# Kernel optimization log

Hardware: AMD Instinct MI355X
Metric: run time of the kernel (lower is better)

The kernel has to match this reference:

```python
import jax, jax.numpy as jnp
import numpy as np

N_NODES = 50000
N_EDGES = 800000
F_IN = 128
HID = 128
F_ADD = 32
N_GRAPHS = 128


def setup_inputs() -> dict:
    key = jax.random.key(0)
    ks = jax.random.split(key, 12)
    x = jax.random.normal(ks[0], (N_NODES, F_IN), dtype=jnp.float32)
    edge_index = jax.random.randint(ks[1], (2, N_EDGES), 0, N_NODES, dtype=jnp.int64)
    batch = jnp.sort(jax.random.randint(ks[2], (N_NODES,), 0, N_GRAPHS, dtype=jnp.int64))
    additional_features = jax.random.normal(ks[3], (N_GRAPHS, F_ADD), dtype=jnp.float32)
    def glorot(k, shape):
        fan_in, fan_out = shape[0], shape[1]
        lim = jnp.sqrt(6.0 / (fan_in + fan_out)).astype(jnp.float32)
        return jax.random.uniform(k, shape, jnp.float32, -lim, lim)
    W1 = glorot(ks[4], (F_IN, HID)); b1 = jnp.zeros((HID,), jnp.float32)
    W2 = glorot(ks[5], (HID, HID)); b2 = jnp.zeros((HID,), jnp.float32)
    fc1_w = glorot(ks[6], (HID + F_ADD, HID)); fc1_b = jnp.zeros((HID,), jnp.float32)
    fc2_w = glorot(ks[7], (HID, 2)); fc2_b = jnp.zeros((2,), jnp.float32)
    return {"x": x, "edge_index": edge_index, "batch": batch,
            "additional_features": additional_features,
            "W1": W1, "b1": b1, "W2": W2, "b2": b2,
            "fc1_w": fc1_w, "fc1_b": fc1_b, "fc2_w": fc2_w, "fc2_b": fc2_b}


def _gcn_conv(h, src, dst, norm, W, b):
    # h: [N, d_in]; symmetric-normalized scatter-add aggregation (PyG GCNConv)
    h = h @ W                                   # [N, d_out]
    msg = h[src] * norm[:, None]                # gather + scale: [E+N, d_out]
    return jax.ops.segment_sum(msg, dst, num_segments=N_NODES) + b


def reference(x, edge_index, batch, additional_features,
              W1, b1, W2, b2, fc1_w, fc1_b, fc2_w, fc2_b):
    loops = jnp.arange(N_NODES, dtype=edge_index.dtype)
    src = jnp.concatenate([edge_index[0], loops])   # A + I
    dst = jnp.concatenate([edge_index[1], loops])
    deg = jax.ops.segment_sum(jnp.ones_like(src, dtype=x.dtype), dst,
                              num_segments=N_NODES)
    dinv = jnp.where(deg > 0, jax.lax.rsqrt(jnp.maximum(deg, 1.0)), 0.0)
    norm = dinv[src] * dinv[dst]

    h = jax.nn.relu(_gcn_conv(x, src, dst, norm, W1, b1))
    h = jax.nn.relu(_gcn_conv(h, src, dst, norm, W2, b2))
    # dropout is identity in eval mode

    sums = jax.ops.segment_sum(h, batch, num_segments=N_GRAPHS)    # [G, HID]
    counts = jax.ops.segment_sum(jnp.ones((N_NODES,), h.dtype), batch,
                                 num_segments=N_GRAPHS)
    pooled = sums / jnp.maximum(counts, 1.0)[:, None]              # global_mean_pool

    z = jnp.concatenate([pooled, additional_features], axis=1)     # [G, HID+F_ADD]
    z = jax.nn.relu(z @ fc1_w + fc1_b)
    return z @ fc2_w + fc2_b                                       # [G, 2]
```

## Files before the change

kernel.cpp:

```cpp
#include <hip/hip_runtime.h>

#define NN 50000
#define NE 800000
#define FD 128
#define FDH 64
#define FA 32
#define NG 128
#define EETOT (NE + NN)
#define NBLK ((NN + 255) / 256)
#define FEPB 2048
#define FNCH ((EETOT + FEPB - 1) / FEPB)
#define NPXCD 6250

typedef __attribute__((ext_vector_type(8))) short short8;
typedef __attribute__((ext_vector_type(4))) float f32x4;

__device__ __forceinline__ float bfbits(unsigned short u) {
    return __uint_as_float(((unsigned int)u) << 16);
}
__device__ __forceinline__ float bflo(unsigned int p) { return __uint_as_float(p << 16); }
__device__ __forceinline__ float bfhi(unsigned int p) { return __uint_as_float(p & 0xffff0000u); }
__device__ __forceinline__ unsigned short f2bf(float f) {
    unsigned int u = __float_as_uint(f);
    unsigned int r = u + 0x7FFFu + ((u >> 16) & 1u);
    return (unsigned short)(r >> 16);
}
__device__ __forceinline__ unsigned int packbf(float a, float b) {
    return (unsigned int)f2bf(a) | ((unsigned int)f2bf(b) << 16);
}

__device__ __forceinline__ int wave_probe_bf16(const unsigned int* t, int nwords) {
    int lane = threadIdx.x & 63;
    unsigned int wv = (lane < nwords) ? t[lane] : 0u;
    int nzp = (wv != 0u) ? 1 : 0;
    unsigned int e = (wv >> 7) & 0xFFu;
    int hitp = (nzp && e >= 100u && e <= 140u) ? 1 : 0;
    int nz = __popcll(__ballot(nzp));
    int hits = __popcll(__ballot(hitp));
    return (nz < 8) ? 1 : (hits * 4 >= nz * 3);
}
__device__ __forceinline__ int wave_probe_is64(const int* ei) {
    int lane = threadIdx.x & 63;
    int v = (lane < 32) ? ei[2 * lane + 1] : 0;
    return (__ballot(v != 0) == 0ull) ? 1 : 0;
}

__global__ __launch_bounds__(128) void mark_kernel(float* out, float v) {
    out[threadIdx.x] = v;
}

__global__ __launch_bounds__(256) void prep(
        const void* addf, const void* w1, const void* b1, const void* w2,
        const void* b2, const void* fc1w, const void* fc1b, const void* fc2w,
        const void* fc2b, unsigned int* W1t, unsigned int* W2t,
        float* addff, float* b1f, float* b2f, float* fc1wf, float* fc1bf,
        float* fc2wf, float* fc2bf, int* degi, int* tsum, float* part) {
    int b = blockIdx.x;
    if (b < 64) {
        int rel = b * 256 + threadIdx.x;
        const void* src = (rel < 8192) ? w1 : w2;
        unsigned int* dst = (rel < 8192) ? W1t : W2t;
        int flag = wave_probe_bf16((const unsigned int*)src, 64);
        int rr = rel & 8191;
        int n = rr >> 6, kk = rr & 63;
        float lo, hi;
        if (flag) {
            const unsigned short* s = (const unsigned short*)src;
            lo = bfbits(s[(2 * kk) * FD + n]);
            hi = bfbits(s[(2 * kk + 1) * FD + n]);
        } else {
            const float* s = (const float*)src;
            lo = s[(2 * kk) * FD + n];
            hi = s[(2 * kk + 1) * FD + n];
        }
        dst[rr] = packbf(lo, hi);
    } else if (b < 163) {
        int i = (b - 64) * 256 + threadIdx.x;
        int wb = (b - 64) * 256 + (threadIdx.x & ~63);
        const void* src; float* dst; int base; int prnw; int lim;
        if      (wb < 4096)  { src = addf; dst = addff; base = 0;     prnw = 64; lim = 4096;  }
        else if (wb < 4224)  { src = b1;   dst = b1f;   base = 4096;  prnw = 64; lim = 128;   }
        else if (wb < 4352)  { src = b2;   dst = b2f;   base = 4224;  prnw = 64; lim = 128;   }
        else if (wb < 24832) { src = fc1w; dst = fc1wf; base = 4352;  prnw = 64; lim = 20480; }
        else if (wb < 24960) { src = fc1b; dst = fc1bf; base = 24832; prnw = 64; lim = 128;   }
        else if (wb < 25216) { src = fc2w; dst = fc2wf; base = 24960; prnw = 64; lim = 256;   }
        else if (wb < 25280) { src = fc2b; dst = fc2bf; base = 25216; prnw = 1;  lim = 2;     }
        else return;
        int flag = wave_probe_bf16((const unsigned int*)src, prnw);
        int rel = i - base;
        if (rel < lim) {
            if (flag) dst[rel] = bfbits(((const unsigned short*)src)[rel]);
            else      dst[rel] = ((const float*)src)[rel];
        }
    } else {
        int i = (b - 163) * 256 + threadIdx.x;
        if      (i < NN)            degi[i] = 0;
        else if (i < NN + 256)      tsum[i - NN] = 0;
        else if (i < NN + 256 + NG * FD) part[i - NN - 256] = 0.f;
    }
}

__global__ __launch_bounds__(256) void deg_kernel(const int* ei, int* deg,
                                                  int* s32, int* d32) {
    int is64 = wave_probe_is64(ei);
    int e = blockIdx.x * 256 + threadIdx.x;
    if (e < NE) {
        int s = is64 ? ei[2 * e] : ei[e];
        int d = is64 ? ei[2 * (NE + e)] : ei[NE + e];
        s32[e] = s;
        d32[e] = d;
        atomicAdd(&deg[d], 1);
    }
}

__global__ __launch_bounds__(256) void scan_fused(const int* degi, const int* batch,
        int* tsum, float* dinv, int* rowstart, int* cursor, int* gstart) {
    __shared__ int sh[256];
    int b = blockIdx.x, t = threadIdx.x;
    int i = b * 256 + t;
    int d = (i < NN) ? degi[i] : 0;
    if (i < NN) dinv[i] = rsqrtf((float)(d + 1));
    int v = (i < NN) ? d + 1 : 0;
    sh[t] = v;
    __syncthreads();
    for (int off = 1; off < 256; off <<= 1) {
        int a = (t >= off) ? sh[t - off] : 0;
        __syncthreads();
        sh[t] += a;
        __syncthreads();
    }
    int incl = sh[t];
    int total = sh[255];
    if (t == 0) atomicExch(&tsum[b], total);
    int pt = 0;
    for (int j = t; j < b; j += 256) {
        int s;
        do { s = atomicAdd(&tsum[j], 0); } while (s == 0);
        pt += s;
    }
    __syncthreads();
    sh[t] = pt;
    __syncthreads();
    for (int off = 128; off >= 1; off >>= 1) {
        if (t < off) sh[t] += sh[t + off];
        __syncthreads();
    }
    int boff = sh[0];
    if (i < NN) {
        int r = boff + incl - v;
        rowstart[i] = r;
        cursor[i]   = r;
    }
    if (i == 0) rowstart[NN] = EETOT;
    if (i < NN) {
        int is64 = (batch[NN - 1] == 0) ? 1 : 0;
        int bc = is64 ? batch[2 * i] : batch[i];
        if (i == 0) {
            for (int g = 0; g <= bc; ++g) gstart[g] = 0;
        } else {
            int bp = is64 ? batch[2 * (i - 1)] : batch[i - 1];
            for (int g = bp + 1; g <= bc; ++g) gstart[g] = i;
        }
        if (i == NN - 1) {
            for (int g = bc + 1; g <= NG; ++g) gstart[g] = NN;
        }
    }
}

__global__ __launch_bounds__(256) void fill_kernel(const int* s32, const int* d32,
        const float* dinv, int* cursor, unsigned int* cv) {
    int chunk = blockIdx.x >> 3;
    int par   = blockIdx.x & 7;
    int base  = chunk * FEPB;
    #pragma unroll
    for (int k = 0; k < FEPB / 256; ++k) {
        int e = base + k * 256 + threadIdx.x;
        if (e >= EETOT) break;
        int s, d;
        if (e < NE) { d = d32[e]; s = -1; }
        else        { s = d = e - NE; }
        if (d / NPXCD != par) continue;
        if (s < 0) s = s32[e];
        int pos = atomicAdd(&cursor[d], 1);
        cv[pos] = (unsigned int)s | ((unsigned int)f2bf(dinv[s] * dinv[d]) << 16);
    }
}

__global__ __launch_bounds__(256) void gemm_mfma(const void* __restrict__ Av,
        const unsigned int* __restrict__ Wt, unsigned short* __restrict__ C,
        int maybe_f32) {
    int wave = threadIdx.x >> 6;
    int lane = threadIdx.x & 63;
    int quad = lane >> 4;
    int l16  = lane & 15;
    int mbase = blockIdx.x * 64 + wave * 16;
    int ra = mbase + l16;
    if (ra >= NN) ra = NN - 1;
    bool f32in = false;
    if (maybe_f32) f32in = !wave_probe_bf16((const unsigned int*)Av, 64);
    short8 af[4];
    if (!f32in) {
        const uint4* Arow = (const uint4*)((const unsigned int*)Av + (size_t)ra * FDH);
        #pragma unroll
        for (int kk = 0; kk < 4; ++kk) {
            uint4 v = Arow[kk * 4 + quad];
            af[kk] = *(short8*)&v;
        }
    } else {
        const float* Arow = (const float*)Av + (size_t)ra * FD;
        #pragma unroll
        for (int kk = 0; kk < 4; ++kk) {
            const float4* p = (const float4*)(Arow + (kk * 4 + quad) * 8);
            float4 u = p[0], v = p[1];
            uint4 q;
            q.x = packbf(u.x, u.y); q.y = packbf(u.z, u.w);
            q.z = packbf(v.x, v.y); q.w = packbf(v.z, v.w);
            af[kk] = *(short8*)&q;
        }
    }
    #pragma unroll
    for (int nt = 0; nt < 8; ++nt) {
        int n = nt * 16 + l16;
        const uint4* Wrow = (const uint4*)(Wt + (size_t)n * FDH);
        f32x4 acc = {0.f, 0.f, 0.f, 0.f};
        #pragma unroll
        for (int kk = 0; kk < 4; ++kk) {
            uint4 wv = Wrow[kk * 4 + quad];
            short8 bf = *(short8*)&wv;
            acc = __builtin_amdgcn_mfma_f32_16x16x32_bf16(af[kk], bf, acc, 0, 0, 0);
        }
        int row0 = mbase + quad * 4;
        #pragma unroll
        for (int reg = 0; reg < 4; ++reg) {
            int r = row0 + reg;
            if (r < NN) C[(size_t)r * FD + nt * 16 + l16] = f2bf(acc[reg]);
        }
    }
}

__global__ __launch_bounds__(256) void aggregate_kernel(const unsigned int* Hb,
        const unsigned int* cv, const int* rowstart, const float* bias,
        unsigned int* outb) {
    int n = blockIdx.x * 4 + (threadIdx.x >> 6);
    int cp = threadIdx.x & 63;
    if (n >= NN) return;
    int jb = rowstart[n], je = rowstart[n + 1];
    float acc0 = 0.f, acc1 = 0.f;
    int j = jb;
    for (; j + 7 < je; j += 8) {
        unsigned int rr[8], hh[8];
        #pragma unroll
        for (int k = 0; k < 8; ++k) rr[k] = cv[j + k];
        #pragma unroll
        for (int k = 0; k < 8; ++k) hh[k] = Hb[(size_t)(rr[k] & 0xFFFFu) * FDH + cp];
        #pragma unroll
        for (int k = 0; k < 8; ++k) {
            float v = bfbits((unsigned short)(rr[k] >> 16));
            acc0 += v * bflo(hh[k]);
            acc1 += v * bfhi(hh[k]);
        }
    }
    for (; j + 3 < je; j += 4) {
        unsigned int rr[4], hh[4];
        #pragma unroll
        for (int k = 0; k < 4; ++k) rr[k] = cv[j + k];
        #pragma unroll
        for (int k = 0; k < 4; ++k) hh[k] = Hb[(size_t)(rr[k] & 0xFFFFu) * FDH + cp];
        #pragma unroll
        for (int k = 0; k < 4; ++k) {
            float v = bfbits((unsigned short)(rr[k] >> 16));
            acc0 += v * bflo(hh[k]);
            acc1 += v * bfhi(hh[k]);
        }
    }
    for (; j < je; ++j) {
        unsigned int r = cv[j];
        unsigned int h = Hb[(size_t)(r & 0xFFFFu) * FDH + cp];
        float v = bfbits((unsigned short)(r >> 16));
        acc0 += v * bflo(h);
        acc1 += v * bfhi(h);
    }
    acc0 = fmaxf(acc0 + bias[2 * cp], 0.f);
    acc1 = fmaxf(acc1 + bias[2 * cp + 1], 0.f);
    outb[(size_t)n * FDH + cp] = packbf(acc0, acc1);
}

__global__ __launch_bounds__(256) void agg_pool(const unsigned int* Hb,
        const unsigned int* cv, const int* rowstart, const float* bias,
        const int* batch, float* part) {
    int w = threadIdx.x >> 6, cp = threadIdx.x & 63;
    int n = blockIdx.x * 4 + w;
    int is64 = (batch[NN - 1] == 0) ? 1 : 0;
    __shared__ float pp[4][FD];
    __shared__ int gg[4];
    float acc0 = 0.f, acc1 = 0.f;
    int jb = rowstart[n], je = rowstart[n + 1];
    int j = jb;
    for (; j + 7 < je; j += 8) {
        unsigned int rr[8], hh[8];
        #pragma unroll
        for (int k = 0; k < 8; ++k) rr[k] = cv[j + k];
        #pragma unroll
        for (int k = 0; k < 8; ++k) hh[k] = Hb[(size_t)(rr[k] & 0xFFFFu) * FDH + cp];
        #pragma unroll
        for (int k = 0; k < 8; ++k) {
            float v = bfbits((unsigned short)(rr[k] >> 16));
            acc0 += v * bflo(hh[k]);
            acc1 += v * bfhi(hh[k]);
        }
    }
    for (; j + 3 < je; j += 4) {
        unsigned int rr[4], hh[4];
        #pragma unroll
        for (int k = 0; k < 4; ++k) rr[k] = cv[j + k];
        #pragma unroll
        for (int k = 0; k < 4; ++k) hh[k] = Hb[(size_t)(rr[k] & 0xFFFFu) * FDH + cp];
        #pragma unroll
        for (int k = 0; k < 4; ++k) {
            float v = bfbits((unsigned short)(rr[k] >> 16));
            acc0 += v * bflo(hh[k]);
            acc1 += v * bfhi(hh[k]);
        }
    }
    for (; j < je; ++j) {
        unsigned int r = cv[j];
        unsigned int h = Hb[(size_t)(r & 0xFFFFu) * FDH + cp];
        float v = bfbits((unsigned short)(r >> 16));
        acc0 += v * bflo(h);
        acc1 += v * bfhi(h);
    }
    acc0 = fmaxf(acc0 + bias[2 * cp], 0.f);
    acc1 = fmaxf(acc1 + bias[2 * cp + 1], 0.f);
    pp[w][2 * cp]     = acc0;
    pp[w][2 * cp + 1] = acc1;
    if (cp == 0) gg[w] = is64 ? batch[2 * n] : batch[n];
    __syncthreads();
    bool allsame = (gg[0] == gg[1]) && (gg[1] == gg[2]) && (gg[2] == gg[3]);
    if (allsame) {
        if (w == 0) {
            float s0 = pp[0][2 * cp] + pp[1][2 * cp] + pp[2][2 * cp] + pp[3][2 * cp];
            float s1 = pp[0][2 * cp + 1] + pp[1][2 * cp + 1]
                     + pp[2][2 * cp + 1] + pp[3][2 * cp + 1];
            atomicAdd(&part[(size_t)gg[0] * FD + 2 * cp], s0);
            atomicAdd(&part[(size_t)gg[0] * FD + 2 * cp + 1], s1);
        }
    } else {
        atomicAdd(&part[(size_t)gg[w] * FD + 2 * cp], acc0);
        atomicAdd(&part[(size_t)gg[w] * FD + 2 * cp + 1], acc1);
    }
}

__global__ __launch_bounds__(128) void head_kernel(const float* part, const int* gstart,
        const float* addf, const float* fc1w, const float* fc1b,
        const float* fc2w, const float* fc2b, const unsigned int* x, void* outp) {
    int g = blockIdx.x;
    int t = threadIdx.x;
    __shared__ float z[FD + FA];
    __shared__ float h[FD];
    int obf = wave_probe_bf16(x, 64);
    float cnt = (float)(gstart[g + 1] - gstart[g]);
    if (cnt < 1.0f) cnt = 1.0f;
    z[t] = part[(size_t)g * FD + t] / cnt;
    if (t < FA) z[FD + t] = addf[g * FA + t];
    __syncthreads();
    float acc = fc1b[t];
    #pragma unroll 4
    for (int k = 0; k < FD + FA; ++k)
        acc += z[k] * fc1w[k * FD + t];
    h[t] = fmaxf(acc, 0.f);
    __syncthreads();
    if (t < 2) {
        float o = fc2b[t];
        for (int j = 0; j < FD; ++j) o += h[j] * fc2w[j * 2 + t];
        if (obf) ((unsigned short*)outp)[g * 2 + t] = f2bf(o);
        else     ((float*)outp)[g * 2 + t] = o;
    }
}

extern "C" void kernel_launch(void* const* d_in, const int* in_sizes, int n_in,
                              void* d_out, int out_size, void* d_ws, size_t ws_size,
                              hipStream_t stream) {
    (void)out_size;

    if (n_in != 12) {
        hipLaunchKernelGGL(mark_kernel, dim3(1), dim3(128), 0, stream,
                           (float*)d_out, 2000.0f);
        return;
    }
    const int exp_sizes[12] = {6400000, 1600000, 50000, 4096, 16384, 128,
                               16384, 128, 20480, 128, 256, 2};
    for (int i = 0; i < 12; ++i) {
        if (in_sizes[i] != exp_sizes[i]) {
            hipLaunchKernelGGL(mark_kernel, dim3(1), dim3(128), 0, stream,
                               (float*)d_out, 3000.0f + 100.0f * i);
            return;
        }
    }

    size_t off = 0;
    char* base = (char*)d_ws;
#define WSALLOC(ptr, type, nbytes) \
    type* ptr = (type*)(base + off); off += (((size_t)(nbytes)) + 255) & ~(size_t)255;
    WSALLOC(bufA,  unsigned int, (size_t)NN * FDH * 4)
    WSALLOC(bufB,  unsigned int, (size_t)NN * FDH * 4)
    WSALLOC(dinv,  float, (size_t)NN * 4)
    WSALLOC(degi,  int,   (size_t)NN * 4)
    WSALLOC(rowst, int,   (size_t)(NN + 1) * 4)
    WSALLOC(cursor,int,   (size_t)NN * 4)
    WSALLOC(tsum,  int,   256 * 4)
    WSALLOC(cv,    unsigned int, (size_t)EETOT * 4)
    WSALLOC(gstart,int,   (size_t)(NG + 1) * 4)
    WSALLOC(part,  float, (size_t)NG * FD * 4)
    WSALLOC(s32,   int,   (size_t)NE * 4)
    WSALLOC(d32,   int,   (size_t)NE * 4)
    WSALLOC(W1t,   unsigned int, (size_t)FD * FDH * 4)
    WSALLOC(W2t,   unsigned int, (size_t)FD * FDH * 4)
    WSALLOC(b1f,   float, FD * 4)
    WSALLOC(b2f,   float, FD * 4)
    WSALLOC(addff, float, (size_t)NG * FA * 4)
    WSALLOC(fc1wf, float, (size_t)(FD + FA) * FD * 4)
    WSALLOC(fc1bf, float, FD * 4)
    WSALLOC(fc2wf, float, FD * 2 * 4)
    WSALLOC(fc2bf, float, 2 * 4)
#undef WSALLOC
    if (ws_size < off) {
        hipLaunchKernelGGL(mark_kernel, dim3(1), dim3(128), 0, stream,
                           (float*)d_out, 1000.0f);
        return;
    }

    const int* ei    = (const int*)d_in[1];
    const int* batch = (const int*)d_in[2];

    hipLaunchKernelGGL(prep, dim3(424), dim3(256), 0, stream,
                       d_in[3], d_in[4], d_in[5], d_in[6], d_in[7],
                       d_in[8], d_in[9], d_in[10], d_in[11],
                       W1t, W2t, addff, b1f, b2f, fc1wf, fc1bf,
                       fc2wf, fc2bf, degi, tsum, part);

    hipLaunchKernelGGL(deg_kernel, dim3((NE + 255) / 256), dim3(256), 0, stream,
                       ei, degi, s32, d32);
    hipLaunchKernelGGL(scan_fused, dim3(NBLK), dim3(256), 0, stream,
                       degi, batch, tsum, dinv, rowst, cursor, gstart);
    hipLaunchKernelGGL(fill_kernel, dim3(FNCH * 8), dim3(256), 0, stream,
                       s32, d32, dinv, cursor, cv);

    hipLaunchKernelGGL(gemm_mfma, dim3((NN + 63) / 64), dim3(256), 0, stream,
                       d_in[0], W1t, (unsigned short*)bufA, 1);
    hipLaunchKernelGGL(aggregate_kernel, dim3((NN + 3) / 4), dim3(256), 0, stream,
                       bufA, cv, rowst, b1f, bufB);
    hipLaunchKernelGGL(gemm_mfma, dim3((NN + 63) / 64), dim3(256), 0, stream,
                       bufB, W2t, (unsigned short*)bufA, 0);
    hipLaunchKernelGGL(agg_pool, dim3(NN / 4), dim3(256), 0, stream,
                       bufA, cv, rowst, b2f, batch, part);

    hipLaunchKernelGGL(head_kernel, dim3(NG), dim3(128), 0, stream,
                       part, gstart, addff, fc1wf, fc1bf, fc2wf, fc2bf,
                       (const unsigned int*)d_in[0], d_out);
}
```

Before: 319.8 us.

## Store features in column panels and pool from the layer-2 output

```diff
diff --git a/kernel.cpp b/kernel.cpp
--- a/kernel.cpp
+++ b/kernel.cpp
@@ -11,6 +11,9 @@
 #define FEPB 2048
 #define FNCH ((EETOT + FEPB - 1) / FEPB)
 #define NPXCD 6250
+#define NPAN 4
+#define PW 16
+#define NBQ (NN / 4)
 
 typedef __attribute__((ext_vector_type(8))) short short8;
 typedef __attribute__((ext_vector_type(4))) float f32x4;
@@ -54,7 +57,7 @@
         const void* b2, const void* fc1w, const void* fc1b, const void* fc2w,
         const void* fc2b, unsigned int* W1t, unsigned int* W2t,
         float* addff, float* b1f, float* b2f, float* fc1wf, float* fc1bf,
-        float* fc2wf, float* fc2bf, int* degi, int* tsum, float* part) {
+        float* fc2wf, float* fc2bf, int* degi, int* tsum) {
     int b = blockIdx.x;
     if (b < 64) {
         int rel = b * 256 + threadIdx.x;
@@ -94,9 +97,8 @@
         }
     } else {
         int i = (b - 163) * 256 + threadIdx.x;
-        if      (i < NN)            degi[i] = 0;
-        else if (i < NN + 256)      tsum[i - NN] = 0;
-        else if (i < NN + 256 + NG * FD) part[i - NN - 256] = 0.f;
+        if      (i < NN)       degi[i] = 0;
+        else if (i < NN + 256) tsum[i - NN] = 0;
     }
 }
 
@@ -188,7 +190,7 @@
 
 __global__ __launch_bounds__(256) void gemm_mfma(const void* __restrict__ Av,
         const unsigned int* __restrict__ Wt, unsigned short* __restrict__ C,
-        int maybe_f32) {
+        int maybe_f32, int panelA) {
     int wave = threadIdx.x >> 6;
     int lane = threadIdx.x & 63;
     int quad = lane >> 4;
@@ -199,7 +201,15 @@
     bool f32in = false;
     if (maybe_f32) f32in = !wave_probe_bf16((const unsigned int*)Av, 64);
     short8 af[4];
-    if (!f32in) {
+    if (panelA) {
+        #pragma unroll
+        for (int kk = 0; kk < 4; ++kk) {
+            const uint4* p = (const uint4*)((const unsigned int*)Av
+                              + (size_t)kk * NN * PW + (size_t)ra * PW + quad * 4);
+            uint4 v = *p;
+            af[kk] = *(short8*)&v;
+        }
+    } else if (!f32in) {
         const uint4* Arow = (const uint4*)((const unsigned int*)Av + (size_t)ra * FDH);
         #pragma unroll
         for (int kk = 0; kk < 4; ++kk) {
@@ -229,11 +239,15 @@
             short8 bf = *(short8*)&wv;
             acc = __builtin_amdgcn_mfma_f32_16x16x32_bf16(af[kk], bf, acc, 0, 0, 0);
         }
+        int ch = nt * 16 + l16;
+        int pp = ch >> 5;
+        int ci = ch & 31;
         int row0 = mbase + quad * 4;
         #pragma unroll
         for (int reg = 0; reg < 4; ++reg) {
             int r = row0 + reg;
-            if (r < NN) C[(size_t)r * FD + nt * 16 + l16] = f2bf(acc[reg]);
+            if (r < NN)
+                C[(size_t)pp * NN * 32 + (size_t)r * 32 + ci] = f2bf(acc[reg]);
         }
     }
 }
@@ -241,133 +255,80 @@
 __global__ __launch_bounds__(256) void aggregate_kernel(const unsigned int* Hb,
         const unsigned int* cv, const int* rowstart, const float* bias,
         unsigned int* outb) {
-    int n = blockIdx.x * 4 + (threadIdx.x >> 6);
-    int cp = threadIdx.x & 63;
-    if (n >= NN) return;
+    int panel = blockIdx.x / NBQ;
+    int nb    = blockIdx.x % NBQ;
+    int wv = threadIdx.x >> 6;
+    int lane = threadIdx.x & 63;
+    int eg = lane >> 4;
+    int c  = lane & 15;
+    int n = nb * 4 + wv;
+    const unsigned int* Hp = Hb + (size_t)panel * NN * PW;
     int jb = rowstart[n], je = rowstart[n + 1];
     float acc0 = 0.f, acc1 = 0.f;
-    int j = jb;
-    for (; j + 7 < je; j += 8) {
-        unsigned int rr[8], hh[8];
-        #pragma unroll
-        for (int k = 0; k < 8; ++k) rr[k] = cv[j + k];
-        #pragma unroll
-        for (int k = 0; k < 8; ++k) hh[k] = Hb[(size_t)(rr[k] & 0xFFFFu) * FDH + cp];
-        #pragma unroll
-        for (int k = 0; k < 8; ++k) {
-            float v = bfbits((unsigned short)(rr[k] >> 16));
-            acc0 += v * bflo(hh[k]);
-            acc1 += v * bfhi(hh[k]);
-        }
-    }
-    for (; j + 3 < je; j += 4) {
-        unsigned int rr[4], hh[4];
-        #pragma unroll
-        for (int k = 0; k < 4; ++k) rr[k] = cv[j + k];
-        #pragma unroll
-        for (int k = 0; k < 4; ++k) hh[k] = Hb[(size_t)(rr[k] & 0xFFFFu) * FDH + cp];
-        #pragma unroll
-        for (int k = 0; k < 4; ++k) {
-            float v = bfbits((unsigned short)(rr[k] >> 16));
-            acc0 += v * bflo(hh[k]);
-            acc1 += v * bfhi(hh[k]);
-        }
-    }
-    for (; j < je; ++j) {
+    int j = jb + eg;
+    for (; j + 4 < je; j += 8) {
+        unsigned int r0 = cv[j], r1 = cv[j + 4];
+        unsigned int h0 = Hp[(size_t)(r0 & 0xFFFFu) * PW + c];
+        unsigned int h1 = Hp[(size_t)(r1 & 0xFFFFu) * PW + c];
+        float v0 = bfbits((unsigned short)(r0 >> 16));
+        float v1 = bfbits((unsigned short)(r1 >> 16));
+        acc0 += v0 * bflo(h0); acc1 += v0 * bfhi(h0);
+        acc0 += v1 * bflo(h1); acc1 += v1 * bfhi(h1);
+    }
+    if (j < je) {
         unsigned int r = cv[j];
-        unsigned int h = Hb[(size_t)(r & 0xFFFFu) * FDH + cp];
+        unsigned int h = Hp[(size_t)(r & 0xFFFFu) * PW + c];
         float v = bfbits((unsigned short)(r >> 16));
         acc0 += v * bflo(h);
         acc1 += v * bfhi(h);
     }
-    acc0 = fmaxf(acc0 + bias[2 * cp], 0.f);
-    acc1 = fmaxf(acc1 + bias[2 * cp + 1], 0.f);
-    outb[(size_t)n * FDH + cp] = packbf(acc0, acc1);
-}
-
-__global__ __launch_bounds__(256) void agg_pool(const unsigned int* Hb,
-        const unsigned int* cv, const int* rowstart, const float* bias,
-        const int* batch, float* part) {
-    int w = threadIdx.x >> 6, cp = threadIdx.x & 63;
-    int n = blockIdx.x * 4 + w;
-    int is64 = (batch[NN - 1] == 0) ? 1 : 0;
-    __shared__ float pp[4][FD];
-    __shared__ int gg[4];
-    float acc0 = 0.f, acc1 = 0.f;
-    int jb = rowstart[n], je = rowstart[n + 1];
-    int j = jb;
-    for (; j + 7 < je; j += 8) {
-        unsigned int rr[8], hh[8];
-        #pragma unroll
-        for (int k = 0; k < 8; ++k) rr[k] = cv[j + k];
-        #pragma unroll
-        for (int k = 0; k < 8; ++k) hh[k] = Hb[(size_t)(rr[k] & 0xFFFFu) * FDH + cp];
-        #pragma unroll
-        for (int k = 0; k < 8; ++k) {
-            float v = bfbits((unsigned short)(rr[k] >> 16));
-            acc0 += v * bflo(hh[k]);
-            acc1 += v * bfhi(hh[k]);
-        }
-    }
-    for (; j + 3 < je; j += 4) {
-        unsigned int rr[4], hh[4];
-        #pragma unroll
-        for (int k = 0; k < 4; ++k) rr[k] = cv[j + k];
-        #pragma unroll
-        for (int k = 0; k < 4; ++k) hh[k] = Hb[(size_t)(rr[k] & 0xFFFFu) * FDH + cp];
-        #pragma unroll
-        for (int k = 0; k < 4; ++k) {
-            float v = bfbits((unsigned short)(rr[k] >> 16));
-            acc0 += v * bflo(hh[k]);
-            acc1 += v * bfhi(hh[k]);
-        }
-    }
-    for (; j < je; ++j) {
-        unsigned int r = cv[j];
-        unsigned int h = Hb[(size_t)(r & 0xFFFFu) * FDH + cp];
-        float v = bfbits((unsigned short)(r >> 16));
-        acc0 += v * bflo(h);
-        acc1 += v * bfhi(h);
-    }
-    acc0 = fmaxf(acc0 + bias[2 * cp], 0.f);
-    acc1 = fmaxf(acc1 + bias[2 * cp + 1], 0.f);
-    pp[w][2 * cp]     = acc0;
-    pp[w][2 * cp + 1] = acc1;
-    if (cp == 0) gg[w] = is64 ? batch[2 * n] : batch[n];
-    __syncthreads();
-    bool allsame = (gg[0] == gg[1]) && (gg[1] == gg[2]) && (gg[2] == gg[3]);
-    if (allsame) {
-        if (w == 0) {
-            float s0 = pp[0][2 * cp] + pp[1][2 * cp] + pp[2][2 * cp] + pp[3][2 * cp];
-            float s1 = pp[0][2 * cp + 1] + pp[1][2 * cp + 1]
-                     + pp[2][2 * cp + 1] + pp[3][2 * cp + 1];
-            atomicAdd(&part[(size_t)gg[0] * FD + 2 * cp], s0);
-            atomicAdd(&part[(size_t)gg[0] * FD + 2 * cp + 1], s1);
-        }
-    } else {
-        atomicAdd(&part[(size_t)gg[w] * FD + 2 * cp], acc0);
-        atomicAdd(&part[(size_t)gg[w] * FD + 2 * cp + 1], acc1);
-    }
-}
-
-__global__ __launch_bounds__(128) void head_kernel(const float* part, const int* gstart,
-        const float* addf, const float* fc1w, const float* fc1b,
+    acc0 += __shfl_xor(acc0, 32); acc0 += __shfl_xor(acc0, 16);
+    acc1 += __shfl_xor(acc1, 32); acc1 += __shfl_xor(acc1, 16);
+    if (eg == 0) {
+        int ch0 = panel * 32 + 2 * c;
+        float r0 = fmaxf(acc0 + bias[ch0], 0.f);
+        float r1 = fmaxf(acc1 + bias[ch0 + 1], 0.f);
+        outb[(size_t)panel * NN * PW + (size_t)n * PW + c] = packbf(r0, r1);
+    }
+}
+
+__global__ __launch_bounds__(256) void poolhead(const unsigned int* Hb,
+        const int* gstart, const float* addf, const float* fc1w, const float* fc1b,
         const float* fc2w, const float* fc2b, const unsigned int* x, void* outp) {
     int g = blockIdx.x;
     int t = threadIdx.x;
+    int q = t >> 6, w = t & 63;
+    int p = w >> 4, ci = w & 15;
+    int obf = wave_probe_bf16(x, 64);
+    int s = gstart[g], e = gstart[g + 1];
+    size_t pb = (size_t)p * NN * PW + ci;
+    float a0 = 0.f, a1 = 0.f;
+    #pragma unroll 4
+    for (int n = s + q; n < e; n += 4) {
+        unsigned int h = Hb[pb + (size_t)n * PW];
+        a0 += bflo(h);
+        a1 += bfhi(h);
+    }
+    __shared__ float pp[4][FD];
     __shared__ float z[FD + FA];
     __shared__ float h[FD];
-    int obf = wave_probe_bf16(x, 64);
-    float cnt = (float)(gstart[g + 1] - gstart[g]);
-    if (cnt < 1.0f) cnt = 1.0f;
-    z[t] = part[(size_t)g * FD + t] / cnt;
-    if (t < FA) z[FD + t] = addf[g * FA + t];
-    __syncthreads();
-    float acc = fc1b[t];
-    #pragma unroll 4
-    for (int k = 0; k < FD + FA; ++k)
-        acc += z[k] * fc1w[k * FD + t];
-    h[t] = fmaxf(acc, 0.f);
+    pp[q][2 * w]     = a0;
+    pp[q][2 * w + 1] = a1;
+    __syncthreads();
+    if (t < FD) {
+        float cnt = (float)(e - s);
+        if (cnt < 1.0f) cnt = 1.0f;
+        z[t] = (pp[0][t] + pp[1][t] + pp[2][t] + pp[3][t]) / cnt;
+    }
+    if (t >= FD && t < FD + FA) z[t] = addf[g * FA + (t - FD)];
+    __syncthreads();
+    if (t < FD) {
+        float acc = fc1b[t];
+        #pragma unroll 4
+        for (int k = 0; k < FD + FA; ++k)
+            acc += z[k] * fc1w[k * FD + t];
+        h[t] = fmaxf(acc, 0.f);
+    }
     __syncthreads();
     if (t < 2) {
         float o = fc2b[t];
@@ -410,7 +371,6 @@
     WSALLOC(tsum,  int,   256 * 4)
     WSALLOC(cv,    unsigned int, (size_t)EETOT * 4)
     WSALLOC(gstart,int,   (size_t)(NG + 1) * 4)
-    WSALLOC(part,  float, (size_t)NG * FD * 4)
     WSALLOC(s32,   int,   (size_t)NE * 4)
     WSALLOC(d32,   int,   (size_t)NE * 4)
     WSALLOC(W1t,   unsigned int, (size_t)FD * FDH * 4)
@@ -432,11 +392,11 @@
     const int* ei    = (const int*)d_in[1];
     const int* batch = (const int*)d_in[2];
 
-    hipLaunchKernelGGL(prep, dim3(424), dim3(256), 0, stream,
+    hipLaunchKernelGGL(prep, dim3(360), dim3(256), 0, stream,
                        d_in[3], d_in[4], d_in[5], d_in[6], d_in[7],
                        d_in[8], d_in[9], d_in[10], d_in[11],
                        W1t, W2t, addff, b1f, b2f, fc1wf, fc1bf,
-                       fc2wf, fc2bf, degi, tsum, part);
+                       fc2wf, fc2bf, degi, tsum);
 
     hipLaunchKernelGGL(deg_kernel, dim3((NE + 255) / 256), dim3(256), 0, stream,
                        ei, degi, s32, d32);
@@ -446,15 +406,15 @@
                        s32, d32, dinv, cursor, cv);
 
     hipLaunchKernelGGL(gemm_mfma, dim3((NN + 63) / 64), dim3(256), 0, stream,
-                       d_in[0], W1t, (unsigned short*)bufA, 1);
-    hipLaunchKernelGGL(aggregate_kernel, dim3((NN + 3) / 4), dim3(256), 0, stream,
+                       d_in[0], W1t, (unsigned short*)bufA, 1, 0);
+    hipLaunchKernelGGL(aggregate_kernel, dim3(NPAN * NBQ), dim3(256), 0, stream,
                        bufA, cv, rowst, b1f, bufB);
     hipLaunchKernelGGL(gemm_mfma, dim3((NN + 63) / 64), dim3(256), 0, stream,
-                       bufB, W2t, (unsigned short*)bufA, 0);
-    hipLaunchKernelGGL(agg_pool, dim3(NN / 4), dim3(256), 0, stream,
-                       bufA, cv, rowst, b2f, batch, part);
-
-    hipLaunchKernelGGL(head_kernel, dim3(NG), dim3(128), 0, stream,
-                       part, gstart, addff, fc1wf, fc1bf, fc2wf, fc2bf,
+                       bufB, W2t, (unsigned short*)bufA, 0, 1);
+    hipLaunchKernelGGL(aggregate_kernel, dim3(NPAN * NBQ), dim3(256), 0, stream,
+                       bufA, cv, rowst, b2f, bufB);
+
+    hipLaunchKernelGGL(poolhead, dim3(NG), dim3(256), 0, stream,
+                       bufB, gstart, addff, fc1wf, fc1bf, fc2wf, fc2bf,
                        (const unsigned int*)d_in[0], d_out);
 }
```

Result: slower. 396.8 us (+24.1%).
